# Performance work log

Hardware: AMD Instinct MI355X
Metric: run time of the kernel (lower is better)

Reference implementation:

```python
import jax, jax.numpy as jnp
import numpy as np

NUM_HEADS = 4
EPS = 1e-5


def setup_inputs() -> dict:
    key = jax.random.key(0)
    ks = jax.random.split(key, 5)
    B, C, H, W = 1, 128, 64, 64
    x = jax.random.normal(ks[0], (B, C, H, W), dtype=jnp.float32)
    # 1x1 conv weights [out_c, in_c]; scaled ~ kaiming-ish to keep softmax non-degenerate
    s = 1.0 / np.sqrt(C)
    qw = jax.random.normal(ks[1], (C, C), dtype=jnp.float32) * s
    kw = jax.random.normal(ks[2], (C, C), dtype=jnp.float32) * s
    vw = jax.random.normal(ks[3], (C, C), dtype=jnp.float32) * s
    pw = jax.random.normal(ks[4], (C, C), dtype=jnp.float32) * s
    zeros = jnp.zeros((C,), dtype=jnp.float32)
    return {
        "x": x,
        "gn_w": jnp.ones((C,), dtype=jnp.float32),
        "gn_b": zeros,
        "qw": qw, "qb": zeros,
        "kw": kw, "kb": zeros,
        "vw": vw, "vb": zeros,
        "pw": pw, "pb": zeros,
    }


def reference(x, gn_w, gn_b, qw, qb, kw, kb, vw, vb, pw, pb):
    B, C, H, W = x.shape
    N = H * W
    d = C // NUM_HEADS

    # GroupNorm(num_groups=1): normalize over (C,H,W) per sample, per-channel affine
    mean = jnp.mean(x, axis=(1, 2, 3), keepdims=True)
    var = jnp.var(x, axis=(1, 2, 3), keepdims=True)
    h = (x - mean) * jax.lax.rsqrt(var + EPS)
    h = h * gn_w[None, :, None, None] + gn_b[None, :, None, None]

    hf = h.reshape(B, C, N)  # [B,C,N]

    def conv1x1(w, b):  # 1x1 conv == channel GEMM
        return jnp.einsum('oc,bcn->bon', w, hf) + b[None, :, None]

    q = conv1x1(qw, qb).reshape(B, NUM_HEADS, d, N)
    k = conv1x1(kw, kb).reshape(B, NUM_HEADS, d, N)
    v = conv1x1(vw, vb).reshape(B, NUM_HEADS, d, N)

    scale = d ** (-0.5)
    attn = jnp.einsum('bhdn,bhdm->bhnm', q, k) * scale  # [B,H,N,N]
    attn = jax.nn.softmax(attn, axis=-1)
    out = jnp.einsum('bhnm,bhdm->bhdn', attn, v)  # [B,H,d,N]

    out = out.reshape(B, C, N)
    out = jnp.einsum('oc,bcn->bon', pw, out) + pb[None, :, None]
    return x + out.reshape(B, C, H, W)
```

## Files before the change

### kernel.cpp

```cpp
#include <hip/hip_runtime.h>

#define NPOS 4096
#define NCH  128
#define NTOT (NPOS * NCH)
#define NHEAD 4
#define DH    32
#define NSPLIT 8
#define KSPAN (NPOS / NSPLIT)
#define NTILE (KSPAN / 64)

typedef __attribute__((ext_vector_type(8))) short short8;
typedef __attribute__((ext_vector_type(4))) float floatx4;
typedef unsigned short u16;
typedef unsigned int   u32;

__device__ __forceinline__ u16 f2bf(float f) {
  u32 u = __float_as_uint(f);
  u += 0x7fffu + ((u >> 16) & 1u);
  return (u16)(u >> 16);
}
__device__ __forceinline__ u32 pack2bf(float a, float b) {
  return (u32)f2bf(a) | ((u32)f2bf(b) << 16);
}
__device__ __forceinline__ u32 pack2bf_fast(float a, float b) {
  return ((__float_as_uint(a) + 0x8000u) >> 16) |
         ((__float_as_uint(b) + 0x8000u) & 0xffff0000u);
}
__device__ __forceinline__ float bf2f(u16 h) {
  return __uint_as_float(((u32)h) << 16);
}

__global__ __launch_bounds__(256) void gn_prep_k(const float* __restrict__ x,
                                                 float2* __restrict__ partials,
                                                 u32* __restrict__ bounds,
                                                 const float* __restrict__ qw, const float* __restrict__ kw,
                                                 const float* __restrict__ vw, const float* __restrict__ pw,
                                                 u16* __restrict__ wq, u16* __restrict__ wk,
                                                 u16* __restrict__ wv, u16* __restrict__ wp) {
  int i = blockIdx.x * 256 + threadIdx.x;
  int w = threadIdx.x >> 6, lane = threadIdx.x & 63;
  float4 a = ((const float4*)x)[i];
  float s  = a.x + a.y + a.z + a.w;
  float sq = a.x*a.x + a.y*a.y + a.z*a.z + a.w*a.w;
#pragma unroll
  for (int m = 1; m < 64; m <<= 1) {
    s  += __shfl_xor(s, m);
    sq += __shfl_xor(sq, m);
  }
  __shared__ float red[8];
  if (lane == 0) { red[w] = s; red[4 + w] = sq; }
  __syncthreads();
  if (threadIdx.x == 0)
    partials[blockIdx.x] = make_float2(red[0]+red[1]+red[2]+red[3],
                                       red[4]+red[5]+red[6]+red[7]);
  if (blockIdx.x == 0 && threadIdx.x < 4) bounds[threadIdx.x] = 0;
  if (blockIdx.x < 16) {
    int t = blockIdx.x * 256 + threadIdx.x;
    const float sc = 0.17677669529663687f * 1.4426950408889634f;
    float4 v = ((const float4*)qw)[t];
    ((uint2*)wq)[t] = make_uint2(pack2bf(v.x*sc, v.y*sc), pack2bf(v.z*sc, v.w*sc));
    v = ((const float4*)kw)[t];
    ((uint2*)wk)[t] = make_uint2(pack2bf(v.x, v.y), pack2bf(v.z, v.w));
    v = ((const float4*)vw)[t];
    ((uint2*)wv)[t] = make_uint2(pack2bf(v.x, v.y), pack2bf(v.z, v.w));
    v = ((const float4*)pw)[t];
    ((uint2*)wp)[t] = make_uint2(pack2bf(v.x, v.y), pack2bf(v.z, v.w));
  }
}

__global__ __launch_bounds__(768) void qkv_k(const float* __restrict__ x,
    const float* __restrict__ gw, const float* __restrict__ gb,
    const float2* __restrict__ partials,
    const u16* __restrict__ wq, const u16* __restrict__ wk, const u16* __restrict__ wv,
    const float* __restrict__ qb, const float* __restrict__ kb, const float* __restrict__ vb,
    u16* __restrict__ q, u16* __restrict__ k, u16* __restrict__ v, u32* __restrict__ bounds) {
  const int t = threadIdx.x;
  const int w = t >> 6, lane = t & 63;
  const int l16 = lane & 15, quad = lane >> 4;
  const int n0 = blockIdx.x * 16;
  const floatx4 zero = {0.f, 0.f, 0.f, 0.f};

  __shared__ float red[16];
  __shared__ float2 swb[128];
  __shared__ __align__(16) u16 hs[16][136];

  if (t < 512) {
    float2 p = partials[t];
    float s = p.x, sq = p.y;
#pragma unroll
    for (int m = 1; m < 64; m <<= 1) {
      s  += __shfl_xor(s, m);
      sq += __shfl_xor(sq, m);
    }
    if (lane == 0) { red[w] = s; red[8 + w] = sq; }
  }
  __syncthreads();
  float mean = (red[0]+red[1]+red[2]+red[3]+red[4]+red[5]+red[6]+red[7]) * (1.0f / NTOT);
  float var  = (red[8]+red[9]+red[10]+red[11]+red[12]+red[13]+red[14]+red[15]) * (1.0f / NTOT)
               - mean * mean;
  float rstd = rsqrtf(var + 1e-5f);
  if (t < 128) {
    float swv = gw[t] * rstd;
    swb[t] = make_float2(swv, gb[t] - mean * swv);
  }
  __syncthreads();
  if (t < 512) {
    int c = t >> 2, seg = t & 3;
    float4 xv = *(const float4*)(x + (size_t)c * NPOS + n0 + seg * 4);
    float2 sb = swb[c];
    int nl = seg * 4;
    hs[nl + 0][c] = f2bf(xv.x * sb.x + sb.y);
    hs[nl + 1][c] = f2bf(xv.y * sb.x + sb.y);
    hs[nl + 2][c] = f2bf(xv.z * sb.x + sb.y);
    hs[nl + 3][c] = f2bf(xv.w * sb.x + sb.y);
  }
  __syncthreads();

  short8 bfr[4];
#pragma unroll
  for (int kk = 0; kk < 4; kk++)
    bfr[kk] = *(const short8*)&hs[l16][kk * 32 + quad * 8];

  const int mat = w >> 2, head = w & 3, ow = head * 32;
  const u16* wm = (mat == 0) ? wq : (mat == 1) ? wk : wv;
  floatx4 a0 = zero, a1 = zero;
  const u16* ap = wm + (size_t)(ow + l16) * NCH + quad * 8;
#pragma unroll
  for (int kk = 0; kk < 4; kk++) {
    a0 = __builtin_amdgcn_mfma_f32_16x16x32_bf16(*(const short8*)(ap + kk*32),          bfr[kk], a0, 0,0,0);
    a1 = __builtin_amdgcn_mfma_f32_16x16x32_bf16(*(const short8*)(ap + 16*NCH + kk*32), bfr[kk], a1, 0,0,0);
  }
  const int n = n0 + l16;
  if (mat == 0) {
    const float sc = 0.17677669529663687f * 1.4426950408889634f;
    u16* qp = q + (size_t)(head * NPOS + n) * DH;
#pragma unroll
    for (int ss = 0; ss < 2; ss++) {
      floatx4 acc = ss ? a1 : a0;
      int od = ss * 16 + quad * 4;
      float r0 = acc[0] + qb[ow+od+0]*sc, r1 = acc[1] + qb[ow+od+1]*sc;
      float r2 = acc[2] + qb[ow+od+2]*sc, r3 = acc[3] + qb[ow+od+3]*sc;
      *(uint2*)(qp + od) = make_uint2(pack2bf(r0, r1), pack2bf(r2, r3));
    }
  } else if (mat == 1) {
    float sumsq = 0.f;
    u16* kp = k + (size_t)(head * NPOS + n) * DH;
#pragma unroll
    for (int ss = 0; ss < 2; ss++) {
      floatx4 acc = ss ? a1 : a0;
      int od = ss * 16 + quad * 4;
      float r0 = acc[0] + kb[ow+od+0], r1 = acc[1] + kb[ow+od+1];
      float r2 = acc[2] + kb[ow+od+2], r3 = acc[3] + kb[ow+od+3];
      sumsq += r0*r0 + r1*r1 + r2*r2 + r3*r3;
      *(uint2*)(kp + od) = make_uint2(pack2bf(r0, r1), pack2bf(r2, r3));
    }
    sumsq += __shfl_xor(sumsq, 16);
    sumsq += __shfl_xor(sumsq, 32);
#pragma unroll
    for (int m = 1; m < 16; m <<= 1) sumsq = fmaxf(sumsq, __shfl_xor(sumsq, m));
    if (lane == 0) atomicMax(&bounds[head], __float_as_uint(sumsq));
  } else {
    u16* vp = v + (size_t)(head * DH) * NPOS + n;
#pragma unroll
    for (int ss = 0; ss < 2; ss++) {
      floatx4 acc = ss ? a1 : a0;
      int od = ss * 16 + quad * 4;
#pragma unroll
      for (int r = 0; r < 4; r++)
        vp[(size_t)(od + r) * NPOS] = f2bf(acc[r] + vb[ow + od + r]);
    }
  }
}

__global__ __launch_bounds__(256, 2) void attn_k(const u16* __restrict__ q, const u16* __restrict__ k,
                                                 const u16* __restrict__ v, const u32* __restrict__ bounds,
                                                 u32* __restrict__ Opair, float* __restrict__ lpart) {
  const int w = threadIdx.x >> 6, lane = threadIdx.x & 63;
  const int l16 = lane & 15, quad = lane >> 4;
  const int s    = blockIdx.x & 7;
  const int i    = blockIdx.x >> 3;
  const int head = i & 3;
  const int q0w  = (i >> 2) * 256 + w * 64;

  float kmax = sqrtf(__uint_as_float(bounds[head])) * 1.0005f;

  short8 bq[4];
  floatx4 cb[4];
#pragma unroll
  for (int qf = 0; qf < 4; qf++) {
    bq[qf] = *(const short8*)(q + (size_t)(head * NPOS + q0w + qf * 16 + l16) * DH + quad * 8);
    float qn2 = 0.f;
#pragma unroll
    for (int j = 0; j < 8; j++) { float f = bf2f((u16)bq[qf][j]); qn2 += f * f; }
    qn2 += __shfl_xor(qn2, 16);
    qn2 += __shfl_xor(qn2, 32);
    float nb = -sqrtf(qn2) * kmax;
    cb[qf][0] = nb; cb[qf][1] = nb; cb[qf][2] = nb; cb[qf][3] = nb;
  }

  floatx4 o0[4], o1[4], ol[4];
#pragma unroll
  for (int qf = 0; qf < 4; qf++) {
    o0[qf] = (floatx4){0,0,0,0}; o1[qf] = (floatx4){0,0,0,0}; ol[qf] = (floatx4){0,0,0,0};
  }
  short8 ones;
#pragma unroll
  for (int j = 0; j < 8; j++) ones[j] = (short)0x3F80;

  const int ko0 = (l16 >> 2) * 8 + (l16 & 3);
  const u16* kbase  = k + (size_t)head * NPOS * DH + (size_t)(s * KSPAN + ko0) * DH + quad * 8;
  const u16* vbase0 = v + (size_t)(head * DH + l16) * NPOS + s * KSPAN + quad * 8;
  const u16* vbase1 = vbase0 + (size_t)16 * NPOS;

  short8 akA[4], avA[4], akB[4], avB[4];

  auto loadT = [&](short8* ak, short8* av, int it) {
    const u16* kb = kbase + it * 2048;
    ak[0] = *(const short8*)(kb);
    ak[1] = *(const short8*)(kb + 128);
    ak[2] = *(const short8*)(kb + 1024);
    ak[3] = *(const short8*)(kb + 1152);
    const u16* v0 = vbase0 + it * 64;
    const u16* v1 = vbase1 + it * 64;
    av[0] = *(const short8*)(v0);
    av[1] = *(const short8*)(v1);
    av[2] = *(const short8*)(v0 + 32);
    av[3] = *(const short8*)(v1 + 32);
  };

  auto compute = [&](const short8* ak, const short8* av) {
#pragma unroll
    for (int qf = 0; qf < 4; qf++) {
      floatx4 c0 = __builtin_amdgcn_mfma_f32_16x16x32_bf16(ak[0], bq[qf], cb[qf], 0, 0, 0);
      floatx4 c1 = __builtin_amdgcn_mfma_f32_16x16x32_bf16(ak[1], bq[qf], cb[qf], 0, 0, 0);
      floatx4 c2 = __builtin_amdgcn_mfma_f32_16x16x32_bf16(ak[2], bq[qf], cb[qf], 0, 0, 0);
      floatx4 c3 = __builtin_amdgcn_mfma_f32_16x16x32_bf16(ak[3], bq[qf], cb[qf], 0, 0, 0);
      {
        float p0 = __builtin_amdgcn_exp2f(c0[0]), p1 = __builtin_amdgcn_exp2f(c0[1]);
        float p2 = __builtin_amdgcn_exp2f(c0[2]), p3 = __builtin_amdgcn_exp2f(c0[3]);
        float p4 = __builtin_amdgcn_exp2f(c1[0]), p5 = __builtin_amdgcn_exp2f(c1[1]);
        float p6 = __builtin_amdgcn_exp2f(c1[2]), p7 = __builtin_amdgcn_exp2f(c1[3]);
        uint4 uu = make_uint4(pack2bf_fast(p0, p1), pack2bf_fast(p2, p3),
                              pack2bf_fast(p4, p5), pack2bf_fast(p6, p7));
        short8 pa = *(short8*)&uu;
        o0[qf] = __builtin_amdgcn_mfma_f32_16x16x32_bf16(pa, av[0], o0[qf], 0, 0, 0);
        o1[qf] = __builtin_amdgcn_mfma_f32_16x16x32_bf16(pa, av[1], o1[qf], 0, 0, 0);
        ol[qf] = __builtin_amdgcn_mfma_f32_16x16x32_bf16(pa, ones,  ol[qf], 0, 0, 0);
      }
      {
        float p0 = __builtin_amdgcn_exp2f(c2[0]), p1 = __builtin_amdgcn_exp2f(c2[1]);
        float p2 = __builtin_amdgcn_exp2f(c2[2]), p3 = __builtin_amdgcn_exp2f(c2[3]);
        float p4 = __builtin_amdgcn_exp2f(c3[0]), p5 = __builtin_amdgcn_exp2f(c3[1]);
        float p6 = __builtin_amdgcn_exp2f(c3[2]), p7 = __builtin_amdgcn_exp2f(c3[3]);
        uint4 uu = make_uint4(pack2bf_fast(p0, p1), pack2bf_fast(p2, p3),
                              pack2bf_fast(p4, p5), pack2bf_fast(p6, p7));
        short8 pa = *(short8*)&uu;
        o0[qf] = __builtin_amdgcn_mfma_f32_16x16x32_bf16(pa, av[2], o0[qf], 0, 0, 0);
        o1[qf] = __builtin_amdgcn_mfma_f32_16x16x32_bf16(pa, av[3], o1[qf], 0, 0, 0);
        ol[qf] = __builtin_amdgcn_mfma_f32_16x16x32_bf16(pa, ones,  ol[qf], 0, 0, 0);
      }
    }
  };

  loadT(akA, avA, 0);
#pragma unroll
  for (int it = 0; it < NTILE; it++) {
    if ((it & 1) == 0) {
      if (it + 1 < NTILE) loadT(akB, avB, it + 1);
      compute(akA, avA);
    } else {
      if (it + 1 < NTILE) loadT(akA, avA, it + 1);
      compute(akB, avB);
    }
  }

  u32*   op = Opair + (size_t)(s * NHEAD + head) * NPOS * 16;
  float* lp = lpart + (size_t)(s * NHEAD + head) * NPOS;
#pragma unroll
  for (int qf = 0; qf < 4; qf++) {
#pragma unroll
    for (int r = 0; r < 4; r++) {
      int qq = q0w + qf * 16 + quad * 4 + r;
      op[(size_t)qq * 16 + l16] = pack2bf(o0[qf][r], o1[qf][r]);
      if (l16 == 0) lp[qq] = ol[qf][r];
    }
  }
}

__global__ __launch_bounds__(512) void proj_k(const u32* __restrict__ Opair,
                                              const float* __restrict__ lpart,
                                              const u16* __restrict__ wp,
                                              const float* __restrict__ pb,
                                              const float* __restrict__ x,
                                              float* __restrict__ out) {
  const int t = threadIdx.x;
  const int w = t >> 6, lane = t & 63;
  const int l16 = lane & 15, quad = lane >> 4;
  const int n0 = blockIdx.x * 16;
  const floatx4 zero = {0.f, 0.f, 0.f, 0.f};
  __shared__ __align__(16) u16 at_lds[16][136];

  {
    const int n = t & 15, ci = t >> 4;
    const int c0 = ci * 4, head = c0 >> 5, off = c0 & 31;
    const int half = off >> 4, j0 = off & 15;
    float acc[4] = {0.f, 0.f, 0.f, 0.f};
    float l = 0.f;
#pragma unroll
    for (int s2 = 0; s2 < NSPLIT; s2++) {
      const u32* pp = Opair + ((size_t)(s2 * NHEAD + head) * NPOS + n0 + n) * 16 + j0;
      uint4 u = *(const uint4*)pp;
      u32 uu[4] = {u.x, u.y, u.z, u.w};
#pragma unroll
      for (int j = 0; j < 4; j++)
        acc[j] += half ? __uint_as_float(uu[j] & 0xffff0000u)
                       : __uint_as_float(uu[j] << 16);
      l += lpart[(size_t)(s2 * NHEAD + head) * NPOS + n0 + n];
    }
    float inv = 1.0f / fmaxf(l, 1e-30f);
    *(uint2*)&at_lds[n][c0] = make_uint2(pack2bf(acc[0]*inv, acc[1]*inv),
                                         pack2bf(acc[2]*inv, acc[3]*inv));
  }
  __syncthreads();

  short8 bfr[4];
#pragma unroll
  for (int kk = 0; kk < 4; kk++)
    bfr[kk] = *(const short8*)&at_lds[l16][kk * 32 + quad * 8];
  const int ow = w * 16;
  floatx4 a0 = zero;
  const u16* ap = wp + (size_t)(ow + l16) * NCH + quad * 8;
#pragma unroll
  for (int kk = 0; kk < 4; kk++)
    a0 = __builtin_amdgcn_mfma_f32_16x16x32_bf16(*(const short8*)(ap + kk*32), bfr[kk], a0, 0,0,0);
  const int n = n0 + l16;
#pragma unroll
  for (int r = 0; r < 4; r++) {
    int o = ow + quad * 4 + r;
    size_t idx = (size_t)o * NPOS + n;
    out[idx] = a0[r] + pb[o] + x[idx];
  }
}

extern "C" void kernel_launch(void* const* d_in, const int* in_sizes, int n_in,
                              void* d_out, int out_size, void* d_ws, size_t ws_size,
                              hipStream_t stream) {
  const float* x   = (const float*)d_in[0];
  const float* gnw = (const float*)d_in[1];
  const float* gnb = (const float*)d_in[2];
  const float* qw  = (const float*)d_in[3];
  const float* qb  = (const float*)d_in[4];
  const float* kw  = (const float*)d_in[5];
  const float* kb  = (const float*)d_in[6];
  const float* vw  = (const float*)d_in[7];
  const float* vb  = (const float*)d_in[8];
  const float* pw  = (const float*)d_in[9];
  const float* pb  = (const float*)d_in[10];
  float* out = (float*)d_out;

  char* wsb = (char*)d_ws;
  float2* partials = (float2*)wsb;
  u32*    bounds   = (u32*)(wsb + 4096);
  u16* wqb = (u16*)(wsb + 8192);
  u16* wkb = wqb + 16384;
  u16* wvb = wkb + 16384;
  u16* wpb = wvb + 16384;
  u16* qbuf = wpb + 16384;
  u16* kbuf = qbuf + NTOT;
  u16* vbuf = kbuf + NTOT;
  u32* Opair = (u32*)(vbuf + NTOT);
  float* lpart = (float*)(Opair + (size_t)NSPLIT * NHEAD * NPOS * 16);

  gn_prep_k<<<512, 256, 0, stream>>>(x, partials, bounds, qw, kw, vw, pw,
                                     wqb, wkb, wvb, wpb);
  qkv_k<<<256, 768, 0, stream>>>(x, gnw, gnb, partials, wqb, wkb, wvb,
                                 qb, kb, vb, qbuf, kbuf, vbuf, bounds);
  attn_k<<<64 * NSPLIT, 256, 0, stream>>>(qbuf, kbuf, vbuf, bounds, Opair, lpart);
  proj_k<<<256, 512, 0, stream>>>(Opair, lpart, wpb, pb, x, out);
}
```

Before: 117.1 us.

## Fuse four stage kernels into one cooperative kernel with grid syncs

Replaces the four separate launches (groupnorm stats, QKV projection, split attention, reduction plus output projection) with a single cooperative kernel of 512 blocks that separates the stages with grid.sync(). The aim is to remove per-launch overhead and the idle gaps between kernels. In exchange, the QKV stage now runs with 256 threads per block and a different role split, and every grid barrier costs time. If the cooperative launch fails, the code falls back to the original four launches.

```diff
diff --git a/kernel.cpp b/kernel.cpp
--- a/kernel.cpp
+++ b/kernel.cpp
@@ -1,4 +1,7 @@
 #include <hip/hip_runtime.h>
+#include <hip/hip_cooperative_groups.h>
+
+namespace cg = cooperative_groups;
 
 #define NPOS 4096
 #define NCH  128
@@ -29,6 +32,7 @@
 __device__ __forceinline__ float bf2f(u16 h) {
   return __uint_as_float(((u32)h) << 16);
 }
+
 
 __global__ __launch_bounds__(256) void gn_prep_k(const float* __restrict__ x,
                                                  float2* __restrict__ partials,
@@ -342,6 +346,327 @@
   }
 }
 
+__global__ __launch_bounds__(256, 2) void mega_k(
+    const float* __restrict__ x,
+    const float* __restrict__ gnw, const float* __restrict__ gnb,
+    const float* __restrict__ qw, const float* __restrict__ qbias,
+    const float* __restrict__ kw, const float* __restrict__ kbias,
+    const float* __restrict__ vw, const float* __restrict__ vbias,
+    const float* __restrict__ pw, const float* __restrict__ pbias,
+    float2* __restrict__ partials, u32* __restrict__ bounds,
+    u16* __restrict__ wq, u16* __restrict__ wk, u16* __restrict__ wv, u16* __restrict__ wp,
+    u16* __restrict__ qb_, u16* __restrict__ kb_, u16* __restrict__ vb_,
+    u32* __restrict__ Opair, float* __restrict__ lpart,
+    float* __restrict__ out) {
+  cg::grid_group grid = cg::this_grid();
+  const int b = blockIdx.x;
+  const int t = threadIdx.x;
+  const int w = t >> 6, lane = t & 63;
+  const int l16 = lane & 15, quad = lane >> 4;
+  const floatx4 zero = {0.f, 0.f, 0.f, 0.f};
+
+  __shared__ float red[8];
+  __shared__ float2 swb[128];
+  __shared__ __align__(16) u16 hs[16][136];
+
+  {
+    int i = b * 256 + t;
+    float4 a = ((const float4*)x)[i];
+    float s  = a.x + a.y + a.z + a.w;
+    float sq = a.x*a.x + a.y*a.y + a.z*a.z + a.w*a.w;
+#pragma unroll
+    for (int m = 1; m < 64; m <<= 1) {
+      s  += __shfl_xor(s, m);
+      sq += __shfl_xor(sq, m);
+    }
+    if (lane == 0) { red[w] = s; red[4 + w] = sq; }
+    __syncthreads();
+    if (t == 0)
+      partials[b] = make_float2(red[0]+red[1]+red[2]+red[3],
+                                red[4]+red[5]+red[6]+red[7]);
+    if (b == 0 && t < 4) bounds[t] = 0;
+    if (b < 16) {
+      int tt = b * 256 + t;
+      const float sc = 0.17677669529663687f * 1.4426950408889634f;
+      float4 v = ((const float4*)qw)[tt];
+      ((uint2*)wq)[tt] = make_uint2(pack2bf(v.x*sc, v.y*sc), pack2bf(v.z*sc, v.w*sc));
+      v = ((const float4*)kw)[tt];
+      ((uint2*)wk)[tt] = make_uint2(pack2bf(v.x, v.y), pack2bf(v.z, v.w));
+      v = ((const float4*)vw)[tt];
+      ((uint2*)wv)[tt] = make_uint2(pack2bf(v.x, v.y), pack2bf(v.z, v.w));
+      v = ((const float4*)pw)[tt];
+      ((uint2*)wp)[tt] = make_uint2(pack2bf(v.x, v.y), pack2bf(v.z, v.w));
+    }
+  }
+  grid.sync();
+
+  {
+    const int role = b >> 8;
+    const int n0 = (b & 255) * 16;
+    __syncthreads();
+    {
+      float2 pa = partials[t], pb2 = partials[t + 256];
+      float s = pa.x + pb2.x, sq = pa.y + pb2.y;
+#pragma unroll
+      for (int m = 1; m < 64; m <<= 1) {
+        s  += __shfl_xor(s, m);
+        sq += __shfl_xor(sq, m);
+      }
+      if (lane == 0) { red[w] = s; red[4 + w] = sq; }
+    }
+    __syncthreads();
+    float mean = (red[0]+red[1]+red[2]+red[3]) * (1.0f / NTOT);
+    float var  = (red[4]+red[5]+red[6]+red[7]) * (1.0f / NTOT) - mean * mean;
+    float rstd = rsqrtf(var + 1e-5f);
+    if (t < 128) {
+      float swv = gnw[t] * rstd;
+      swb[t] = make_float2(swv, gnb[t] - mean * swv);
+    }
+    __syncthreads();
+#pragma unroll
+    for (int i = t; i < 512; i += 256) {
+      int c = i >> 2, seg = i & 3;
+      float4 xv = *(const float4*)(x + (size_t)c * NPOS + n0 + seg * 4);
+      float2 sb = swb[c];
+      int nl = seg * 4;
+      hs[nl + 0][c] = f2bf(xv.x * sb.x + sb.y);
+      hs[nl + 1][c] = f2bf(xv.y * sb.x + sb.y);
+      hs[nl + 2][c] = f2bf(xv.z * sb.x + sb.y);
+      hs[nl + 3][c] = f2bf(xv.w * sb.x + sb.y);
+    }
+    __syncthreads();
+
+    short8 bfr[4];
+#pragma unroll
+    for (int kk = 0; kk < 4; kk++)
+      bfr[kk] = *(const short8*)&hs[l16][kk * 32 + quad * 8];
+
+    const int head = w, ow = head * 32;
+    const int n = n0 + l16;
+    if (role == 0) {
+      {
+        floatx4 a0 = zero, a1 = zero;
+        const u16* ap = wq + (size_t)(ow + l16) * NCH + quad * 8;
+#pragma unroll
+        for (int kk = 0; kk < 4; kk++) {
+          a0 = __builtin_amdgcn_mfma_f32_16x16x32_bf16(*(const short8*)(ap + kk*32),          bfr[kk], a0, 0,0,0);
+          a1 = __builtin_amdgcn_mfma_f32_16x16x32_bf16(*(const short8*)(ap + 16*NCH + kk*32), bfr[kk], a1, 0,0,0);
+        }
+        const float sc = 0.17677669529663687f * 1.4426950408889634f;
+        u16* qp = qb_ + (size_t)(head * NPOS + n) * DH;
+#pragma unroll
+        for (int ss = 0; ss < 2; ss++) {
+          floatx4 acc = ss ? a1 : a0;
+          int od = ss * 16 + quad * 4;
+          float r0 = acc[0] + qbias[ow+od+0]*sc, r1 = acc[1] + qbias[ow+od+1]*sc;
+          float r2 = acc[2] + qbias[ow+od+2]*sc, r3 = acc[3] + qbias[ow+od+3]*sc;
+          *(uint2*)(qp + od) = make_uint2(pack2bf(r0, r1), pack2bf(r2, r3));
+        }
+      }
+      {
+        floatx4 a0 = zero, a1 = zero;
+        const u16* ap = wv + (size_t)(ow + l16) * NCH + quad * 8;
+#pragma unroll
+        for (int kk = 0; kk < 4; kk++) {
+          a0 = __builtin_amdgcn_mfma_f32_16x16x32_bf16(*(const short8*)(ap + kk*32),          bfr[kk], a0, 0,0,0);
+          a1 = __builtin_amdgcn_mfma_f32_16x16x32_bf16(*(const short8*)(ap + 16*NCH + kk*32), bfr[kk], a1, 0,0,0);
+        }
+        u16* vp = vb_ + (size_t)(head * DH) * NPOS + n;
+#pragma unroll
+        for (int ss = 0; ss < 2; ss++) {
+          floatx4 acc = ss ? a1 : a0;
+          int od = ss * 16 + quad * 4;
+#pragma unroll
+          for (int r = 0; r < 4; r++)
+            vp[(size_t)(od + r) * NPOS] = f2bf(acc[r] + vbias[ow + od + r]);
+        }
+      }
+    } else {
+      floatx4 a0 = zero, a1 = zero;
+      const u16* ap = wk + (size_t)(ow + l16) * NCH + quad * 8;
+#pragma unroll
+      for (int kk = 0; kk < 4; kk++) {
+        a0 = __builtin_amdgcn_mfma_f32_16x16x32_bf16(*(const short8*)(ap + kk*32),          bfr[kk], a0, 0,0,0);
+        a1 = __builtin_amdgcn_mfma_f32_16x16x32_bf16(*(const short8*)(ap + 16*NCH + kk*32), bfr[kk], a1, 0,0,0);
+      }
+      float sumsq = 0.f;
+      u16* kp = kb_ + (size_t)(head * NPOS + n) * DH;
+#pragma unroll
+      for (int ss = 0; ss < 2; ss++) {
+        floatx4 acc = ss ? a1 : a0;
+        int od = ss * 16 + quad * 4;
+        float r0 = acc[0] + kbias[ow+od+0], r1 = acc[1] + kbias[ow+od+1];
+        float r2 = acc[2] + kbias[ow+od+2], r3 = acc[3] + kbias[ow+od+3];
+        sumsq += r0*r0 + r1*r1 + r2*r2 + r3*r3;
+        *(uint2*)(kp + od) = make_uint2(pack2bf(r0, r1), pack2bf(r2, r3));
+      }
+      sumsq += __shfl_xor(sumsq, 16);
+      sumsq += __shfl_xor(sumsq, 32);
+#pragma unroll
+      for (int m = 1; m < 16; m <<= 1) sumsq = fmaxf(sumsq, __shfl_xor(sumsq, m));
+      if (lane == 0) atomicMax(&bounds[head], __float_as_uint(sumsq));
+    }
+  }
+  grid.sync();
+
+  {
+    const int s    = b & 7;
+    const int i    = b >> 3;
+    const int head = i & 3;
+    const int q0w  = (i >> 2) * 256 + w * 64;
+
+    float kmax = sqrtf(__uint_as_float(bounds[head])) * 1.0005f;
+
+    short8 bq[4];
+    floatx4 cbv[4];
+#pragma unroll
+    for (int qf = 0; qf < 4; qf++) {
+      bq[qf] = *(const short8*)(qb_ + (size_t)(head * NPOS + q0w + qf * 16 + l16) * DH + quad * 8);
+      float qn2 = 0.f;
+#pragma unroll
+      for (int j = 0; j < 8; j++) { float f = bf2f((u16)bq[qf][j]); qn2 += f * f; }
+      qn2 += __shfl_xor(qn2, 16);
+      qn2 += __shfl_xor(qn2, 32);
+      float nb = -sqrtf(qn2) * kmax;
+      cbv[qf][0] = nb; cbv[qf][1] = nb; cbv[qf][2] = nb; cbv[qf][3] = nb;
+    }
+
+    floatx4 o0[4], o1[4], ol[4];
+#pragma unroll
+    for (int qf = 0; qf < 4; qf++) { o0[qf] = zero; o1[qf] = zero; ol[qf] = zero; }
+    short8 ones;
+#pragma unroll
+    for (int j = 0; j < 8; j++) ones[j] = (short)0x3F80;
+
+    const int ko0 = (l16 >> 2) * 8 + (l16 & 3);
+    const u16* kbase  = kb_ + (size_t)head * NPOS * DH + (size_t)(s * KSPAN + ko0) * DH + quad * 8;
+    const u16* vbase0 = vb_ + (size_t)(head * DH + l16) * NPOS + s * KSPAN + quad * 8;
+    const u16* vbase1 = vbase0 + (size_t)16 * NPOS;
+
+    short8 akA[4], avA[4], akB[4], avB[4];
+
+    auto loadT = [&](short8* ak, short8* av, int it) {
+      const u16* kb = kbase + it * 2048;
+      ak[0] = *(const short8*)(kb);
+      ak[1] = *(const short8*)(kb + 128);
+      ak[2] = *(const short8*)(kb + 1024);
+      ak[3] = *(const short8*)(kb + 1152);
+      const u16* v0 = vbase0 + it * 64;
+      const u16* v1 = vbase1 + it * 64;
+      av[0] = *(const short8*)(v0);
+      av[1] = *(const short8*)(v1);
+      av[2] = *(const short8*)(v0 + 32);
+      av[3] = *(const short8*)(v1 + 32);
+    };
+
+    auto compute = [&](const short8* ak, const short8* av) {
+#pragma unroll
+      for (int qf = 0; qf < 4; qf++) {
+        floatx4 c0 = __builtin_amdgcn_mfma_f32_16x16x32_bf16(ak[0], bq[qf], cbv[qf], 0, 0, 0);
+        floatx4 c1 = __builtin_amdgcn_mfma_f32_16x16x32_bf16(ak[1], bq[qf], cbv[qf], 0, 0, 0);
+        floatx4 c2 = __builtin_amdgcn_mfma_f32_16x16x32_bf16(ak[2], bq[qf], cbv[qf], 0, 0, 0);
+        floatx4 c3 = __builtin_amdgcn_mfma_f32_16x16x32_bf16(ak[3], bq[qf], cbv[qf], 0, 0, 0);
+        {
+          float p0 = __builtin_amdgcn_exp2f(c0[0]), p1 = __builtin_amdgcn_exp2f(c0[1]);
+          float p2 = __builtin_amdgcn_exp2f(c0[2]), p3 = __builtin_amdgcn_exp2f(c0[3]);
+          float p4 = __builtin_amdgcn_exp2f(c1[0]), p5 = __builtin_amdgcn_exp2f(c1[1]);
+          float p6 = __builtin_amdgcn_exp2f(c1[2]), p7 = __builtin_amdgcn_exp2f(c1[3]);
+          uint4 uu = make_uint4(pack2bf_fast(p0, p1), pack2bf_fast(p2, p3),
+                                pack2bf_fast(p4, p5), pack2bf_fast(p6, p7));
+          short8 pa = *(short8*)&uu;
+          o0[qf] = __builtin_amdgcn_mfma_f32_16x16x32_bf16(pa, av[0], o0[qf], 0, 0, 0);
+          o1[qf] = __builtin_amdgcn_mfma_f32_16x16x32_bf16(pa, av[1], o1[qf], 0, 0, 0);
+          ol[qf] = __builtin_amdgcn_mfma_f32_16x16x32_bf16(pa, ones,  ol[qf], 0, 0, 0);
+        }
+        {
+          float p0 = __builtin_amdgcn_exp2f(c2[0]), p1 = __builtin_amdgcn_exp2f(c2[1]);
+          float p2 = __builtin_amdgcn_exp2f(c2[2]), p3 = __builtin_amdgcn_exp2f(c2[3]);
+          float p4 = __builtin_amdgcn_exp2f(c3[0]), p5 = __builtin_amdgcn_exp2f(c3[1]);
+          float p6 = __builtin_amdgcn_exp2f(c3[2]), p7 = __builtin_amdgcn_exp2f(c3[3]);
+          uint4 uu = make_uint4(pack2bf_fast(p0, p1), pack2bf_fast(p2, p3),
+                                pack2bf_fast(p4, p5), pack2bf_fast(p6, p7));
+          short8 pa = *(short8*)&uu;
+          o0[qf] = __builtin_amdgcn_mfma_f32_16x16x32_bf16(pa, av[2], o0[qf], 0, 0, 0);
+          o1[qf] = __builtin_amdgcn_mfma_f32_16x16x32_bf16(pa, av[3], o1[qf], 0, 0, 0);
+          ol[qf] = __builtin_amdgcn_mfma_f32_16x16x32_bf16(pa, ones,  ol[qf], 0, 0, 0);
+        }
+      }
+    };
+
+    loadT(akA, avA, 0);
+#pragma unroll
+    for (int it = 0; it < NTILE; it++) {
+      if ((it & 1) == 0) {
+        if (it + 1 < NTILE) loadT(akB, avB, it + 1);
+        compute(akA, avA);
+      } else {
+        if (it + 1 < NTILE) loadT(akA, avA, it + 1);
+        compute(akB, avB);
+      }
+    }
+
+    u32*   op = Opair + (size_t)(s * NHEAD + head) * NPOS * 16;
+    float* lp = lpart + (size_t)(s * NHEAD + head) * NPOS;
+#pragma unroll
+    for (int qf = 0; qf < 4; qf++) {
+#pragma unroll
+      for (int r = 0; r < 4; r++) {
+        int qq = q0w + qf * 16 + quad * 4 + r;
+        op[(size_t)qq * 16 + l16] = pack2bf(o0[qf][r], o1[qf][r]);
+        if (l16 == 0) lp[qq] = ol[qf][r];
+      }
+    }
+  }
+  grid.sync();
+
+  {
+    const int n0 = (b >> 1) * 16;
+    const int half = b & 1;
+    __syncthreads();
+#pragma unroll
+    for (int rep = 0; rep < 2; rep++) {
+      const int n = t & 15, ci = (t >> 4) + rep * 16;
+      const int c0 = ci * 4, head = c0 >> 5, off = c0 & 31;
+      const int hhalf = off >> 4, j0 = off & 15;
+      float acc[4] = {0.f, 0.f, 0.f, 0.f};
+      float l = 0.f;
+#pragma unroll
+      for (int s2 = 0; s2 < NSPLIT; s2++) {
+        const u32* pp = Opair + ((size_t)(s2 * NHEAD + head) * NPOS + n0 + n) * 16 + j0;
+        uint4 u = *(const uint4*)pp;
+        u32 uu[4] = {u.x, u.y, u.z, u.w};
+#pragma unroll
+        for (int j = 0; j < 4; j++)
+          acc[j] += hhalf ? __uint_as_float(uu[j] & 0xffff0000u)
+                          : __uint_as_float(uu[j] << 16);
+        l += lpart[(size_t)(s2 * NHEAD + head) * NPOS + n0 + n];
+      }
+      float inv = 1.0f / fmaxf(l, 1e-30f);
+      *(uint2*)&hs[n][c0] = make_uint2(pack2bf(acc[0]*inv, acc[1]*inv),
+                                       pack2bf(acc[2]*inv, acc[3]*inv));
+    }
+    __syncthreads();
+
+    short8 bfr[4];
+#pragma unroll
+    for (int kk = 0; kk < 4; kk++)
+      bfr[kk] = *(const short8*)&hs[l16][kk * 32 + quad * 8];
+    const int ow = half * 64 + w * 16;
+    floatx4 a0 = zero;
+    const u16* ap = wp + (size_t)(ow + l16) * NCH + quad * 8;
+#pragma unroll
+    for (int kk = 0; kk < 4; kk++)
+      a0 = __builtin_amdgcn_mfma_f32_16x16x32_bf16(*(const short8*)(ap + kk*32), bfr[kk], a0, 0,0,0);
+    const int n = n0 + l16;
+#pragma unroll
+    for (int r = 0; r < 4; r++) {
+      int o = ow + quad * 4 + r;
+      size_t idx = (size_t)o * NPOS + n;
+      out[idx] = a0[r] + pbias[o] + x[idx];
+    }
+  }
+}
+
 extern "C" void kernel_launch(void* const* d_in, const int* in_sizes, int n_in,
                               void* d_out, int out_size, void* d_ws, size_t ws_size,
                               hipStream_t stream) {
@@ -371,10 +696,25 @@
   u32* Opair = (u32*)(vbuf + NTOT);
   float* lpart = (float*)(Opair + (size_t)NSPLIT * NHEAD * NPOS * 16);
 
-  gn_prep_k<<<512, 256, 0, stream>>>(x, partials, bounds, qw, kw, vw, pw,
-                                     wqb, wkb, wvb, wpb);
-  qkv_k<<<256, 768, 0, stream>>>(x, gnw, gnb, partials, wqb, wkb, wvb,
-                                 qb, kb, vb, qbuf, kbuf, vbuf, bounds);
-  attn_k<<<64 * NSPLIT, 256, 0, stream>>>(qbuf, kbuf, vbuf, bounds, Opair, lpart);
-  proj_k<<<256, 512, 0, stream>>>(Opair, lpart, wpb, pb, x, out);
-}
+  void* args[] = {
+    (void*)&x, (void*)&gnw, (void*)&gnb,
+    (void*)&qw, (void*)&qb, (void*)&kw, (void*)&kb,
+    (void*)&vw, (void*)&vb, (void*)&pw, (void*)&pb,
+    (void*)&partials, (void*)&bounds,
+    (void*)&wqb, (void*)&wkb, (void*)&wvb, (void*)&wpb,
+    (void*)&qbuf, (void*)&kbuf, (void*)&vbuf,
+    (void*)&Opair, (void*)&lpart,
+    (void*)&out
+  };
+  hipError_t err = hipLaunchCooperativeKernel((void*)mega_k, dim3(512), dim3(256),
+                                              args, 0, stream);
+  if (err != hipSuccess) {
+    (void)hipGetLastError();
+    gn_prep_k<<<512, 256, 0, stream>>>(x, partials, bounds, qw, kw, vw, pw,
+                                       wqb, wkb, wvb, wpb);
+    qkv_k<<<256, 768, 0, stream>>>(x, gnw, gnb, partials, wqb, wkb, wvb,
+                                   qb, kb, vb, qbuf, kbuf, vbuf, bounds);
+    attn_k<<<64 * NSPLIT, 256, 0, stream>>>(qbuf, kbuf, vbuf, bounds, Opair, lpart);
+    proj_k<<<256, 512, 0, stream>>>(Opair, lpart, wpb, pb, x, out);
+  }
+}
```

Measured after the change: 288.4 us. 146% more time.
